# Kernel tuning notes

Measured on AMD Instinct MI355X. Metric: run time of the kernel, lower is better.

The kernel has to match this reference:

```python
import jax, jax.numpy as jnp
import numpy as np

N = 50000
IN_DIM = 128
HID = 64
HEADS = 4
OUT_DIM = 2
NEG_SLOPE = 0.2


def setup_inputs() -> dict:
    key = jax.random.key(0)
    ks = jax.random.split(key, 10)
    x = jax.random.normal(ks[0], (N, IN_DIM), dtype=jnp.float32)
    edge_index = jax.random.randint(ks[1], (2, 800000), 0, N, dtype=jnp.int64)
    s = 0.1
    W1 = jax.random.normal(ks[2], (IN_DIM, HEADS * HID), dtype=jnp.float32) * s
    att_src1 = jax.random.normal(ks[3], (HEADS, HID), dtype=jnp.float32) * s
    att_dst1 = jax.random.normal(ks[4], (HEADS, HID), dtype=jnp.float32) * s
    b1 = jnp.zeros((HEADS * HID,), dtype=jnp.float32)
    W2 = jax.random.normal(ks[5], (HEADS * HID, 1 * OUT_DIM), dtype=jnp.float32) * s
    att_src2 = jax.random.normal(ks[6], (1, OUT_DIM), dtype=jnp.float32) * s
    att_dst2 = jax.random.normal(ks[7], (1, OUT_DIM), dtype=jnp.float32) * s
    b2 = jnp.zeros((OUT_DIM,), dtype=jnp.float32)
    return {"x": x, "edge_index": edge_index, "W1": W1, "att_src1": att_src1,
            "att_dst1": att_dst1, "b1": b1, "W2": W2, "att_src2": att_src2,
            "att_dst2": att_dst2, "b2": b2}


def gat_conv(x, W, att_src, att_dst, b, src, dst, heads, ch):
    # x: [N, F_in] -> h: [N, H, C]
    n = x.shape[0]
    h = (x @ W).reshape(n, heads, ch)
    a_s = jnp.einsum('nhc,hc->nh', h, att_src)  # [N, H]
    a_d = jnp.einsum('nhc,hc->nh', h, att_dst)  # [N, H]
    e = jax.nn.leaky_relu(a_s[src] + a_d[dst], NEG_SLOPE)  # [E, H]
    # segment softmax over incoming edges of each destination node
    m = jax.ops.segment_max(e, dst, num_segments=n)
    ex = jnp.exp(e - m[dst])
    z = jax.ops.segment_sum(ex, dst, num_segments=n)
    alpha = ex / z[dst]  # [E, H]
    msg = h[src] * alpha[:, :, None]  # [E, H, C]
    out = jax.ops.segment_sum(msg, dst, num_segments=n)  # [N, H, C]
    return out.reshape(n, heads * ch) + b


def reference(x, edge_index, W1, att_src1, att_dst1, b1, W2, att_src2, att_dst2, b2):
    n = x.shape[0]
    loop = jnp.arange(n, dtype=edge_index.dtype)
    src = jnp.concatenate([edge_index[0], loop])  # add_self_loops (PyG default)
    dst = jnp.concatenate([edge_index[1], loop])
    h = gat_conv(x, W1, att_src1, att_dst1, b1, src, dst, HEADS, HID)
    h = jax.nn.elu(h)
    # dropout is identity at inference
    out = gat_conv(h, W2, att_src2, att_dst2, b2, src, dst, 1, OUT_DIM)
    return out
```

## Files before the change

### kernel.cpp

```cpp
#include <hip/hip_runtime.h>

#define NN     50000
#define E_RAW  800000
#define ETOT   (E_RAW + NN)
#define FIN    128
#define FH     256
#define NEG    0.2f
#define BCAP   64

#define P_PART 16
#define DPW    3125
#define R_REP  16
#define EPW    (E_RAW / R_REP)
#define CNT_WGS (P_PART * R_REP)
#define PREP_WGS 8
#define OFF_NB  ((NN + 255) / 256)
#define GEMM_NB ((NN + 63) / 64)

typedef __attribute__((ext_vector_type(8))) short s16x8;
typedef __attribute__((ext_vector_type(4))) float f32x4;

static __device__ __forceinline__ float leaky(float v) { return v > 0.f ? v : NEG * v; }

static __device__ __forceinline__ unsigned short f2bf(float f) {
    unsigned u = __float_as_uint(f);
    unsigned r = u + 0x7fffu + ((u >> 16) & 1u);
    return (unsigned short)(r >> 16);
}

__global__ __launch_bounds__(1024) void k_count(const int* __restrict__ ei,
                                                const float* __restrict__ W1,
                                                unsigned short* __restrict__ Wt_bf,
                                                int* __restrict__ pcnt)
{
    const int t = threadIdx.x;
    if (blockIdx.x >= CNT_WGS) {
        const int base = (blockIdx.x - CNT_WGS) * 4096;
        for (int i = t; i < 4096; i += 1024) {
            int idx = base + i;
            int k = idx >> 8, col = idx & 255;
            Wt_bf[col * FIN + k] = f2bf(W1[k * FH + col]);
        }
        return;
    }
    __shared__ int lcnt[DPW];
    const int p  = blockIdx.x >> 4;
    const int r  = blockIdx.x & 15;
    const int lo = p * DPW;
    for (int i = t; i < DPW; i += 1024) lcnt[i] = 0;
    __syncthreads();
    const int ebase = r * EPW, eend = ebase + EPW;
    for (int e0 = ebase + t * 4; e0 < eend; e0 += 4096) {
        int4 dv4 = *(const int4*)&ei[E_RAW + e0];
#pragma unroll
        for (int k = 0; k < 4; k++) {
            unsigned rel = (unsigned)((&dv4.x)[k] - lo);
            if (rel < DPW) atomicAdd(&lcnt[rel], 1);
        }
    }
    __syncthreads();
    for (int i = t; i < DPW; i += 1024)
        pcnt[r * NN + lo + i] = lcnt[i];
}

__global__ __launch_bounds__(256) void k_gx(const float* __restrict__ x,
                                            const unsigned short* __restrict__ Wt_bf,
                                            const float* __restrict__ att_src,
                                            const float* __restrict__ att_dst,
                                            const int* __restrict__ pcnt,
                                            int* __restrict__ soff,
                                            int* __restrict__ cnt,
                                            int* __restrict__ csr_src,
                                            unsigned short* __restrict__ h1b,
                                            float* __restrict__ a_s,
                                            float* __restrict__ a_d)
{
    const int t = threadIdx.x;
    if (blockIdx.x < OFF_NB) {
        int d = blockIdx.x * 256 + t;
        if (d >= NN) return;
        int run = 1;
#pragma unroll
        for (int r = 0; r < R_REP; r++) {
            soff[r * NN + d] = run;
            run += pcnt[r * NN + d];
        }
        cnt[d] = run;
        csr_src[(size_t)d << 6] = d;
        return;
    }

    __shared__ unsigned short Sbuf[64 * 256];
    const int w    = t >> 6;
    const int lane = t & 63;
    const int li   = lane & 15;
    const int q8   = (lane >> 4) * 8;
    const int quad = lane >> 4;
    const int n0   = (blockIdx.x - OFF_NB) * 64;

    {
        const int node_l = t >> 2;
        const int k0 = (t & 3) * 32;
        int nn = n0 + node_l; if (nn >= NN) nn = NN - 1;
        const float* xp = &x[(size_t)nn * FIN + k0];
        unsigned short* xd = &Sbuf[node_l * 136 + k0];
#pragma unroll
        for (int i = 0; i < 8; i++) {
            float4 v = *(const float4*)&xp[i * 4];
            xd[i * 4 + 0] = f2bf(v.x);
            xd[i * 4 + 1] = f2bf(v.y);
            xd[i * 4 + 2] = f2bf(v.z);
            xd[i * 4 + 3] = f2bf(v.w);
        }
    }
    __syncthreads();

    f32x4 acc[4][4];
#pragma unroll
    for (int i = 0; i < 4; i++)
#pragma unroll
        for (int j = 0; j < 4; j++) acc[i][j] = (f32x4){0.f, 0.f, 0.f, 0.f};

#pragma unroll
    for (int kki = 0; kki < 4; kki++) {
        const int kk = kki * 32;
        s16x8 af[4], bf[4];
#pragma unroll
        for (int n16 = 0; n16 < 4; n16++) {
            int col = w * 64 + n16 * 16 + li;
            bf[n16] = *(const s16x8*)&Wt_bf[col * FIN + kk + q8];
        }
#pragma unroll
        for (int m16 = 0; m16 < 4; m16++)
            af[m16] = *(const s16x8*)&Sbuf[(m16 * 16 + li) * 136 + kk + q8];
#pragma unroll
        for (int m16 = 0; m16 < 4; m16++)
#pragma unroll
            for (int n16 = 0; n16 < 4; n16++)
                acc[m16][n16] = __builtin_amdgcn_mfma_f32_16x16x32_bf16(
                    af[m16], bf[n16], acc[m16][n16], 0, 0, 0);
    }

    {
        float as_c[4], ad_c[4];
#pragma unroll
        for (int n16 = 0; n16 < 4; n16++) {
            int col = w * 64 + n16 * 16 + li;
            as_c[n16] = att_src[col];
            ad_c[n16] = att_dst[col];
        }
#pragma unroll
        for (int m16 = 0; m16 < 4; m16++) {
            float ps[4], pd[4];
#pragma unroll
            for (int reg = 0; reg < 4; reg++) {
                float s = 0.f, d = 0.f;
#pragma unroll
                for (int n16 = 0; n16 < 4; n16++) {
                    s += acc[m16][n16][reg] * as_c[n16];
                    d += acc[m16][n16][reg] * ad_c[n16];
                }
                ps[reg] = s; pd[reg] = d;
            }
#pragma unroll
            for (int off = 1; off < 16; off <<= 1) {
#pragma unroll
                for (int reg = 0; reg < 4; reg++) {
                    ps[reg] += __shfl_xor(ps[reg], off);
                    pd[reg] += __shfl_xor(pd[reg], off);
                }
            }
            if (li == 0) {
#pragma unroll
                for (int reg = 0; reg < 4; reg++) {
                    int node = n0 + m16 * 16 + quad * 4 + reg;
                    if (node < NN) {
                        a_s[node * 4 + w] = ps[reg];
                        a_d[node * 4 + w] = pd[reg];
                    }
                }
            }
        }
    }

    __syncthreads();
#pragma unroll
    for (int m16 = 0; m16 < 4; m16++)
#pragma unroll
        for (int n16 = 0; n16 < 4; n16++)
#pragma unroll
            for (int reg = 0; reg < 4; reg++)
                Sbuf[(m16 * 16 + quad * 4 + reg) * FH + w * 64 + n16 * 16 + li] =
                    f2bf(acc[m16][n16][reg]);
    __syncthreads();
    {
        const int node_l = t >> 2;
        const int c0 = (t & 3) * 64;
        int node = n0 + node_l;
        if (node < NN) {
#pragma unroll
            for (int i = 0; i < 8; i++)
                *(uint4*)&h1b[(size_t)node * FH + c0 + i * 8] =
                    *(const uint4*)&Sbuf[node_l * FH + c0 + i * 8];
        }
    }
}

__global__ __launch_bounds__(1024) void k_scat2(const int* __restrict__ ei,
                                                const int* __restrict__ soff,
                                                int* __restrict__ csr_src)
{
    __shared__ int cur[DPW];
    const int t  = threadIdx.x;
    const int p  = blockIdx.x >> 4;
    const int r  = blockIdx.x & 15;
    const int lo = p * DPW;
    for (int i = t; i < DPW; i += 1024)
        cur[i] = soff[r * NN + lo + i];
    __syncthreads();
    const int ebase = r * EPW, eend = ebase + EPW;
    for (int e0 = ebase + t * 4; e0 < eend; e0 += 4096) {
        int4 sv4 = *(const int4*)&ei[e0];
        int4 dv4 = *(const int4*)&ei[E_RAW + e0];
#pragma unroll
        for (int k = 0; k < 4; k++) {
            int d = (&dv4.x)[k];
            unsigned rel = (unsigned)(d - lo);
            if (rel < DPW) {
                int pos = atomicAdd(&cur[rel], 1);
                if (pos < BCAP)
                    csr_src[((size_t)d << 6) + pos] = (&sv4.x)[k];
            }
        }
    }
}

__global__ __launch_bounds__(256) void k_agg1(const int* __restrict__ cnt,
                                              const int* __restrict__ csr_src,
                                              const float* __restrict__ a_s1,
                                              const float* __restrict__ a_d1,
                                              const unsigned short* __restrict__ h1b,
                                              const float* __restrict__ b1,
                                              const float* __restrict__ W2,
                                              const float* __restrict__ att_src2,
                                              const float* __restrict__ att_dst2,
                                              float4* __restrict__ nd4)
{
    const int lane = threadIdx.x & 63;
    const int n = blockIdx.x * 4 + (threadIdx.x >> 6);
    if (n >= NN) return;
    int m = cnt[n]; if (m > BCAP) m = BCAP;
    const int h = lane >> 4;
    const float ad_h = a_d1[n * 4 + h];
    float acc0 = 0.f, acc1 = 0.f, acc2 = 0.f, acc3 = 0.f, z = 0.f;
    const int* sp = &csr_src[(size_t)n << 6];
#pragma unroll 4
    for (int j = 0; j < m; j++) {
        int s = sp[j];
        float as_h = a_s1[s * 4 + h];
        float ex = __expf(leaky(as_h + ad_h));
        unsigned long long wv =
            *(const unsigned long long*)(h1b + (size_t)s * FH + lane * 4);
        unsigned lo = (unsigned)wv, hi = (unsigned)(wv >> 32);
        acc0 += __uint_as_float(lo << 16) * ex;
        acc1 += __uint_as_float(lo & 0xffff0000u) * ex;
        acc2 += __uint_as_float(hi << 16) * ex;
        acc3 += __uint_as_float(hi & 0xffff0000u) * ex;
        z += ex;
    }
    const int c0 = lane * 4;
    float4 bb = *(const float4*)&b1[c0];
    float v0 = acc0 / z + bb.x;
    float v1 = acc1 / z + bb.y;
    float v2 = acc2 / z + bb.z;
    float v3 = acc3 / z + bb.w;
    v0 = v0 > 0.f ? v0 : __expf(v0) - 1.f;
    v1 = v1 > 0.f ? v1 : __expf(v1) - 1.f;
    v2 = v2 > 0.f ? v2 : __expf(v2) - 1.f;
    v3 = v3 > 0.f ? v3 : __expf(v3) - 1.f;
    float4 w2a = *(const float4*)&W2[c0 * 2];
    float4 w2b = *(const float4*)&W2[c0 * 2 + 4];
    float s0 = v0 * w2a.x + v1 * w2a.z + v2 * w2b.x + v3 * w2b.z;
    float s1 = v0 * w2a.y + v1 * w2a.w + v2 * w2b.y + v3 * w2b.w;
#pragma unroll
    for (int off = 32; off; off >>= 1) {
        s0 += __shfl_xor(s0, off);
        s1 += __shfl_xor(s1, off);
    }
    if (lane == 0) {
        float4 nd;
        nd.x = s0; nd.y = s1;
        nd.z = s0 * att_src2[0] + s1 * att_src2[1];
        nd.w = s0 * att_dst2[0] + s1 * att_dst2[1];
        nd4[n] = nd;
    }
}

__global__ __launch_bounds__(256) void k_agg2(const int* __restrict__ cnt,
                                              const int* __restrict__ csr_src,
                                              const float4* __restrict__ nd4,
                                              const float* __restrict__ b2,
                                              float* __restrict__ out)
{
    const int l = threadIdx.x & 15;
    const int n = blockIdx.x * 16 + (threadIdx.x >> 4);
    if (n >= NN) return;
    int m = cnt[n]; if (m > BCAP) m = BCAP;
    const int* sp = &csr_src[(size_t)n << 6];
    const float ad = nd4[n].w;
    float z = 0.f, a0 = 0.f, a1 = 0.f;
    for (int j = l; j < m; j += 16) {
        int s = sp[j];
        float4 f = nd4[s];
        float ex = __expf(leaky(f.z + ad));
        z  += ex;
        a0 += f.x * ex;
        a1 += f.y * ex;
    }
#pragma unroll
    for (int off = 8; off; off >>= 1) {
        z  += __shfl_xor(z, off);
        a0 += __shfl_xor(a0, off);
        a1 += __shfl_xor(a1, off);
    }
    if (l == 0) {
        out[n * 2 + 0] = a0 / z + b2[0];
        out[n * 2 + 1] = a1 / z + b2[1];
    }
}

extern "C" void kernel_launch(void* const* d_in, const int* in_sizes, int n_in,
                              void* d_out, int out_size, void* d_ws, size_t ws_size,
                              hipStream_t stream)
{
    const float* x        = (const float*)d_in[0];
    const int*   ei       = (const int*)d_in[1];
    const float* W1       = (const float*)d_in[2];
    const float* att_src1 = (const float*)d_in[3];
    const float* att_dst1 = (const float*)d_in[4];
    const float* b1       = (const float*)d_in[5];
    const float* W2       = (const float*)d_in[6];
    const float* att_src2 = (const float*)d_in[7];
    const float* att_dst2 = (const float*)d_in[8];
    const float* b2       = (const float*)d_in[9];
    float* out = (float*)d_out;

    int*    csr_src = (int*)d_ws;
    unsigned short* h1b = (unsigned short*)(csr_src + (size_t)NN * 64);
    unsigned short* Wt_bf = h1b + (size_t)NN * FH;
    int*    pcnt  = (int*)(Wt_bf + FH * FIN);
    int*    soff  = pcnt + (size_t)NN * R_REP;
    int*    cnt   = soff + (size_t)NN * R_REP;
    float*  a_s1  = (float*)(cnt + NN);
    float*  a_d1  = a_s1 + (size_t)NN * 4;
    float4* nd4   = (float4*)(a_d1 + (size_t)NN * 4);

    k_count<<<CNT_WGS + PREP_WGS, 1024, 0, stream>>>(ei, W1, Wt_bf, pcnt);
    k_gx<<<OFF_NB + GEMM_NB, 256, 0, stream>>>(x, Wt_bf, att_src1, att_dst1,
                                               pcnt, soff, cnt, csr_src,
                                               h1b, a_s1, a_d1);
    k_scat2<<<CNT_WGS, 1024, 0, stream>>>(ei, soff, csr_src);
    k_agg1<<<(NN + 3) / 4, 256, 0, stream>>>(cnt, csr_src, a_s1, a_d1, h1b,
                                             b1, W2, att_src2, att_dst2, nd4);
    k_agg2<<<(NN + 15) / 16, 256, 0, stream>>>(cnt, csr_src, nd4, b2, out);
}
```

Measured before the change: 208.7 us.

## Fuse CSR scatter into GEMM kernel with in-block prefix offsets

Folds the separate scatter kernel into the GEMM kernel as extra workgroups. Each scatter block now computes its own per-replica starting offsets from the partial counts, so the soff array and the offset pass disappear. The aim is to drop one kernel launch, remove a round trip through global memory, and let the scatter overlap with the MFMA GEMM. In exchange, scatter blocks run with 256 threads instead of 1024, and every block re-reads all 16 partial counts for its partition, which is redundant work.

```diff
diff --git a/kernel.cpp b/kernel.cpp
--- a/kernel.cpp
+++ b/kernel.cpp
@@ -14,7 +14,7 @@
 #define EPW    (E_RAW / R_REP)
 #define CNT_WGS (P_PART * R_REP)
 #define PREP_WGS 8
-#define OFF_NB  ((NN + 255) / 256)
+#define SC2_NB  (P_PART * R_REP)
 #define GEMM_NB ((NN + 63) / 64)
 
 typedef __attribute__((ext_vector_type(8))) short s16x8;
@@ -67,36 +67,60 @@
                                             const unsigned short* __restrict__ Wt_bf,
                                             const float* __restrict__ att_src,
                                             const float* __restrict__ att_dst,
+                                            const int* __restrict__ ei,
                                             const int* __restrict__ pcnt,
-                                            int* __restrict__ soff,
                                             int* __restrict__ cnt,
                                             int* __restrict__ csr_src,
                                             unsigned short* __restrict__ h1b,
                                             float* __restrict__ a_s,
                                             float* __restrict__ a_d)
 {
+    __shared__ __align__(16) unsigned char SbufRaw[64 * 256 * 2];
     const int t = threadIdx.x;
-    if (blockIdx.x < OFF_NB) {
-        int d = blockIdx.x * 256 + t;
-        if (d >= NN) return;
-        int run = 1;
-#pragma unroll
-        for (int r = 0; r < R_REP; r++) {
-            soff[r * NN + d] = run;
-            run += pcnt[r * NN + d];
-        }
-        cnt[d] = run;
-        csr_src[(size_t)d << 6] = d;
+
+    if (blockIdx.x < SC2_NB) {
+        int* cur = (int*)SbufRaw;
+        const int p  = blockIdx.x >> 4;
+        const int r  = blockIdx.x & 15;
+        const int lo = p * DPW;
+        for (int i = t; i < DPW; i += 256) {
+            int run = 1, tot = 1;
+#pragma unroll
+            for (int rr = 0; rr < R_REP; rr++) {
+                int v = pcnt[rr * NN + lo + i];
+                if (rr < r) run += v;
+                tot += v;
+            }
+            cur[i] = run;
+            if (r == 15) cnt[lo + i] = tot;
+            if (r == 0)  csr_src[(size_t)(lo + i) << 6] = lo + i;
+        }
+        __syncthreads();
+        const int ebase = r * EPW, eend = ebase + EPW;
+        for (int e0 = ebase + t * 4; e0 < eend; e0 += 1024) {
+            int4 sv4 = *(const int4*)&ei[e0];
+            int4 dv4 = *(const int4*)&ei[E_RAW + e0];
+#pragma unroll
+            for (int k = 0; k < 4; k++) {
+                int d = (&dv4.x)[k];
+                unsigned rel = (unsigned)(d - lo);
+                if (rel < DPW) {
+                    int pos = atomicAdd(&cur[rel], 1);
+                    if (pos < BCAP)
+                        csr_src[((size_t)d << 6) + pos] = (&sv4.x)[k];
+                }
+            }
+        }
         return;
     }
 
-    __shared__ unsigned short Sbuf[64 * 256];
+    unsigned short* Sbuf = (unsigned short*)SbufRaw;
     const int w    = t >> 6;
     const int lane = t & 63;
     const int li   = lane & 15;
     const int q8   = (lane >> 4) * 8;
     const int quad = lane >> 4;
-    const int n0   = (blockIdx.x - OFF_NB) * 64;
+    const int n0   = (blockIdx.x - SC2_NB) * 64;
 
     {
         const int node_l = t >> 2;
@@ -202,35 +226,6 @@
             for (int i = 0; i < 8; i++)
                 *(uint4*)&h1b[(size_t)node * FH + c0 + i * 8] =
                     *(const uint4*)&Sbuf[node_l * FH + c0 + i * 8];
-        }
-    }
-}
-
-__global__ __launch_bounds__(1024) void k_scat2(const int* __restrict__ ei,
-                                                const int* __restrict__ soff,
-                                                int* __restrict__ csr_src)
-{
-    __shared__ int cur[DPW];
-    const int t  = threadIdx.x;
-    const int p  = blockIdx.x >> 4;
-    const int r  = blockIdx.x & 15;
-    const int lo = p * DPW;
-    for (int i = t; i < DPW; i += 1024)
-        cur[i] = soff[r * NN + lo + i];
-    __syncthreads();
-    const int ebase = r * EPW, eend = ebase + EPW;
-    for (int e0 = ebase + t * 4; e0 < eend; e0 += 4096) {
-        int4 sv4 = *(const int4*)&ei[e0];
-        int4 dv4 = *(const int4*)&ei[E_RAW + e0];
-#pragma unroll
-        for (int k = 0; k < 4; k++) {
-            int d = (&dv4.x)[k];
-            unsigned rel = (unsigned)(d - lo);
-            if (rel < DPW) {
-                int pos = atomicAdd(&cur[rel], 1);
-                if (pos < BCAP)
-                    csr_src[((size_t)d << 6) + pos] = (&sv4.x)[k];
-            }
         }
     }
 }
@@ -349,17 +344,14 @@
     unsigned short* h1b = (unsigned short*)(csr_src + (size_t)NN * 64);
     unsigned short* Wt_bf = h1b + (size_t)NN * FH;
     int*    pcnt  = (int*)(Wt_bf + FH * FIN);
-    int*    soff  = pcnt + (size_t)NN * R_REP;
-    int*    cnt   = soff + (size_t)NN * R_REP;
+    int*    cnt   = pcnt + (size_t)NN * R_REP;
     float*  a_s1  = (float*)(cnt + NN);
     float*  a_d1  = a_s1 + (size_t)NN * 4;
     float4* nd4   = (float4*)(a_d1 + (size_t)NN * 4);
 
     k_count<<<CNT_WGS + PREP_WGS, 1024, 0, stream>>>(ei, W1, Wt_bf, pcnt);
-    k_gx<<<OFF_NB + GEMM_NB, 256, 0, stream>>>(x, Wt_bf, att_src1, att_dst1,
-                                               pcnt, soff, cnt, csr_src,
-                                               h1b, a_s1, a_d1);
-    k_scat2<<<CNT_WGS, 1024, 0, stream>>>(ei, soff, csr_src);
+    k_gx<<<SC2_NB + GEMM_NB, 256, 0, stream>>>(x, Wt_bf, att_src1, att_dst1, ei,
+                                               pcnt, cnt, csr_src, h1b, a_s1, a_d1);
     k_agg1<<<(NN + 3) / 4, 256, 0, stream>>>(cnt, csr_src, a_s1, a_d1, h1b,
                                              b1, W2, att_src2, att_dst2, nd4);
     k_agg2<<<(NN + 15) / 16, 256, 0, stream>>>(cnt, csr_src, nd4, b2, out);
```

New measurement: 218.6 us. 4.7% more time.
